# Kernel tuning notes

Measured on AMD Instinct MI355X. Metric: run time of the kernel, lower is better.

The kernel has to match this reference:

```python
import jax, jax.numpy as jnp
import numpy as np

PSIZE = 3
PSTRIDE = 3
N = PSIZE * PSTRIDE   # 9 attention tokens
P = PSIZE ** 2        # 9 pixels per token


def setup_inputs() -> dict:
    key = jax.random.key(0)
    k1, k2, k3, k4, k5 = jax.random.split(key, 5)
    B, H, W, C = 8192, 9, 9, 256
    hidden = C // 2
    x = jax.random.normal(k1, (B, H, W, C), dtype=jnp.float32)
    W_fc = jax.random.normal(k2, (hidden, C), dtype=jnp.float32) * (C ** -0.5)
    b_fc = jax.random.normal(k3, (hidden,), dtype=jnp.float32) * 0.01
    block_idx = jax.random.randint(k4, (B,), 0, 1024, dtype=jnp.int32)
    match_vec = jax.random.randint(k5, (1024, 1), 0, 2, dtype=jnp.int32)
    return {"x": x, "W_fc": W_fc, "b_fc": b_fc, "block_idx": block_idx, "match_vec": match_vec}


def reference(x, W_fc, b_fc, block_idx, match_vec):
    B, H, Wd, C = x.shape
    hidden = W_fc.shape[0]
    scale = (hidden * P) ** -0.5

    # [B, pstride, psize, pstride, psize, C] -> patch-major [B, ps, ps, p, p, C]
    xv = x.reshape(B, PSTRIDE, PSIZE, PSTRIDE, PSIZE, C).transpose(0, 1, 3, 2, 4, 5)
    x_fc = xv.reshape(B, N, P, C)

    # linear projection C -> hidden, then flatten pixels: q [B, N, P*hidden]
    q = (jnp.einsum('bnpc,hc->bnph', x_fc, W_fc) + b_fc).reshape(B, N, P * hidden)

    attn = jnp.einsum('bnd,bmd->bnm', q, q) * scale  # [B, N, N]

    # additive mask: -100 on diagonal, zeroed out entirely for matched samples
    base = jnp.where(jnp.eye(N, dtype=bool), jnp.float32(-100.0), jnp.float32(0.0))
    cur_match = match_vec[block_idx].squeeze(-1)  # [B]
    mask = jnp.where(cur_match[:, None, None] == 1, jnp.float32(0.0), base[None])

    attn = jax.nn.softmax(attn + mask, axis=-1)

    v = xv.reshape(B, N, P * C)
    out = attn @ v  # [B, N, P*C]

    out = out.reshape(B, PSTRIDE, PSTRIDE, PSIZE, PSIZE, C)
    out = out.transpose(0, 1, 3, 2, 4, 5).reshape(B, H, Wd, C)
    return out
```

## Files before the change

### kernel.cpp

```cpp
#include <hip/hip_runtime.h>

typedef short short8 __attribute__((ext_vector_type(8)));
typedef float floatx16 __attribute__((ext_vector_type(16)));
typedef float floatx4 __attribute__((ext_vector_type(4)));

#define ROWS 81
#define CDIM 256
#define XT   0
#define QH   41472
#define SC   51840
#define AB   52864
#define TOT  53376

__device__ __forceinline__ unsigned short f2bf(float f) {
    union { float f; unsigned int u; } v; v.f = f;
    return (unsigned short)((v.u + 0x7FFFu + ((v.u >> 16) & 1u)) >> 16);
}

__global__ void wconv_kernel(const float* __restrict__ W,
                             unsigned short* __restrict__ Wb, int n) {
    int i = blockIdx.x * 256 + threadIdx.x;
    if (i < n) Wb[i] = f2bf(W[i]);
}

__global__ __launch_bounds__(512, 6)
void attn_kernel(const float* __restrict__ x,
                 const unsigned short* __restrict__ Wb,
                 const float* __restrict__ b_fc,
                 const int* __restrict__ block_idx,
                 const int* __restrict__ match_vec,
                 float* __restrict__ out)
{
    __shared__ __align__(16) char smem[TOT];
    const int b     = blockIdx.x;
    const int t     = threadIdx.x;
    const int lane  = t & 63;
    const int wave  = t >> 6;
    const int l15   = lane & 15;
    const int kg    = lane >> 4;
    const int l31   = lane & 31;
    const int khalf = lane >> 5;

    int cm = 0;
    if (t < 9) cm = match_vec[block_idx[b]];

    short8 wfrag[8];
    {
        const unsigned short* wr = Wb + (wave * 16 + l15) * CDIM + kg * 8;
#pragma unroll
        for (int ks = 0; ks < 8; ++ks)
            wfrag[ks] = *(const short8*)(wr + ks * 32);
    }
    const float bias = b_fc[wave * 16 + l15];

    if (t < 256) ((float*)(smem + SC))[t] = 0.f;

    {
        const float* xb = x + (size_t)b * (ROWS * CDIM);
        for (int k = t; k < ROWS * 32; k += 512) {
            int gr = k >> 5;
            int c0 = (k & 31) * 8;
            float4 a0 = *(const float4*)(xb + gr * CDIM + c0);
            float4 a1 = *(const float4*)(xb + gr * CDIM + c0 + 4);
            int hh = gr / 9, ww = gr - hh * 9;
            int p = (hh % 3) * 3 + (ww % 3);
            int m = (hh / 3) * 3 + (ww / 3);
            int r = p * 9 + m;
            short8 v;
            v[0] = (short)f2bf(a0.x); v[1] = (short)f2bf(a0.y);
            v[2] = (short)f2bf(a0.z); v[3] = (short)f2bf(a0.w);
            v[4] = (short)f2bf(a1.x); v[5] = (short)f2bf(a1.y);
            v[6] = (short)f2bf(a1.z); v[7] = (short)f2bf(a1.w);
            *(short8*)(smem + XT + r * 512 + ((c0 * 2) ^ ((r & 15) << 4))) = v;
        }
    }
    __syncthreads();

    floatx4 acc[6];
#pragma unroll
    for (int i = 0; i < 6; ++i)
#pragma unroll
        for (int j = 0; j < 4; ++j) acc[i][j] = 0.f;
    const int swl = l15 << 4;
#pragma unroll
    for (int ks = 0; ks < 8; ++ks) {
        int cb = ks * 64 + kg * 16;
#pragma unroll
        for (int tile = 0; tile < 6; ++tile) {
            int r = tile * 16 + l15;
            short8 a = *(const short8*)(smem + XT + r * 512 + (cb ^ swl));
            acc[tile] = __builtin_amdgcn_mfma_f32_16x16x32_bf16(a, wfrag[ks], acc[tile], 0, 0, 0);
        }
    }

    if (wave < 4) {
        int h2 = (wave * 16 + l15) * 2;
#pragma unroll
        for (int tile = 0; tile < 6; ++tile)
#pragma unroll
            for (int reg = 0; reg < 4; ++reg) {
                int r = tile * 16 + kg * 4 + reg;
                if (r < ROWS)
                    *(unsigned short*)(smem + QH + r * 128 + (h2 ^ ((r & 7) << 4))) =
                        f2bf(acc[tile][reg] + bias);
            }
    }
    __syncthreads();

    const int nc = (l15 < 9) ? l15 : 8;
#define GRAM_HALF()                                                                 \
    {                                                                               \
        floatx4 g; g[0] = 0.f; g[1] = 0.f; g[2] = 0.f; g[3] = 0.f;                  \
        for (int ks = wave; ks < 18; ks += 8) {                                     \
            int p  = ks >> 1;                                                       \
            int h0 = (ks & 1) * 64 + kg * 16;           \
            int row = p * 9 + nc;                                                   \
            short8 f = *(const short8*)(smem + QH + row * 128 +                     \
                                        (h0 ^ ((row & 7) << 4)));                   \
            g = __builtin_amdgcn_mfma_f32_16x16x32_bf16(f, f, g, 0, 0, 0);          \
        }                                                                           \
        float* sc = (float*)(smem + SC);                                            \
        _Pragma("unroll")                                                           \
        for (int reg = 0; reg < 4; ++reg)                                           \
            atomicAdd(&sc[(kg * 4 + reg) * 16 + l15], g[reg]);                      \
    }
    GRAM_HALF();
    __syncthreads();

    if (wave >= 4) {
        int h2 = ((wave - 4) * 16 + l15) * 2;
#pragma unroll
        for (int tile = 0; tile < 6; ++tile)
#pragma unroll
            for (int reg = 0; reg < 4; ++reg) {
                int r = tile * 16 + kg * 4 + reg;
                if (r < ROWS)
                    *(unsigned short*)(smem + QH + r * 128 + (h2 ^ ((r & 7) << 4))) =
                        f2bf(acc[tile][reg] + bias);
            }
    }
    __syncthreads();
    GRAM_HALF();
    __syncthreads();

    if (t < 9) {
        const float scale = 0.029462782549439483f;
        float* sc = (float*)(smem + SC);
        float s[9];
        float mx = -1e30f;
#pragma unroll
        for (int m = 0; m < 9; ++m) {
            float v = sc[t * 16 + m] * scale;
            if (m == t && cm != 1) v -= 100.f;
            s[m] = v;
            mx = fmaxf(mx, v);
        }
        float sum = 0.f;
#pragma unroll
        for (int m = 0; m < 9; ++m) { s[m] = __expf(s[m] - mx); sum += s[m]; }
        float inv = 1.f / sum;
        unsigned short* ab = (unsigned short*)(smem + AB) + t * 16;
#pragma unroll
        for (int m = 0; m < 9; ++m) ab[m] = f2bf(s[m] * inv);
#pragma unroll
        for (int m = 9; m < 16; ++m) ab[m] = 0;
    }
    __syncthreads();

    {
        const int n  = l31;
        const int nm = (n < 9) ? n : 0;
        short8 bf = *(const short8*)(smem + AB + nm * 32 + khalf * 16);
        float* ob = out + (size_t)b * (ROWS * CDIM);
        int hh0 = 0, ww0 = 0;
        if (n < 9) { hh0 = (n / 3) * 3; ww0 = (n % 3) * 3; }
#pragma unroll
        for (int tt = 0; tt < 9; ++tt) {
            int tile = wave * 9 + tt;
            int d = tile * 32 + l31;
            int p = d >> 8, c = d & 255;
            short8 af;
#pragma unroll
            for (int j = 0; j < 8; ++j) {
                int mm = khalf * 8 + j; if (mm > 8) mm = 8;
                int row = p * 9 + mm;
                af[j] = *(const short*)(smem + XT + row * 512 + ((c * 2) ^ ((row & 15) << 4)));
            }
            floatx16 dacc;
#pragma unroll
            for (int i = 0; i < 16; ++i) dacc[i] = 0.f;
            dacc = __builtin_amdgcn_mfma_f32_32x32x16_bf16(af, bf, dacc, 0, 0, 0);
            if (n < 9) {
#pragma unroll
                for (int q2 = 0; q2 < 4; ++q2) {
                    int d0 = tile * 32 + q2 * 8 + khalf * 4;
                    int p0 = d0 >> 8, c0 = d0 & 255;
                    int gr = (hh0 + p0 / 3) * 9 + (ww0 + p0 % 3);
                    *(float4*)(ob + gr * CDIM + c0) =
                        make_float4(dacc[q2 * 4 + 0], dacc[q2 * 4 + 1],
                                    dacc[q2 * 4 + 2], dacc[q2 * 4 + 3]);
                }
            }
        }
    }
}

extern "C" void kernel_launch(void* const* d_in, const int* in_sizes, int n_in,
                              void* d_out, int out_size, void* d_ws, size_t ws_size,
                              hipStream_t stream) {
    const float* x    = (const float*)d_in[0];
    const float* W    = (const float*)d_in[1];
    const float* bfc  = (const float*)d_in[2];
    const int*   bidx = (const int*)d_in[3];
    const int*   mvec = (const int*)d_in[4];
    float* outp = (float*)d_out;
    unsigned short* Wb = (unsigned short*)d_ws;

    int nW = in_sizes[1];
    wconv_kernel<<<(nW + 255) / 256, 256, 0, stream>>>(W, Wb, nW);

    int B = in_sizes[0] / (ROWS * CDIM);
    attn_kernel<<<B, 512, 0, stream>>>(x, Wb, bfc, bidx, mvec, outp);
}
```

Before: 417.3 us.

## Store full Q tile at once, split Gram into per-wave partials, change swizzle

Enlarges the Q shared-memory region so all 8 waves write their projection results at once, removing the two-phase write/Gram sequence and two barriers. The Gram matrix is now computed by 4 waves, each writing its own partial buffer; the softmax thread sums the four partials, replacing the shared-memory atomics. The X-tile swizzle gains an extra XOR term to reduce bank conflicts, and the launch-bounds occupancy hint drops from 6 to 2 because shared-memory use per block grows to about 70 KB. Fewer blocks may fit per CU, which could reduce latency hiding in exchange for fewer barriers.

```diff
diff --git a/kernel.cpp b/kernel.cpp
--- a/kernel.cpp
+++ b/kernel.cpp
@@ -7,10 +7,12 @@
 #define ROWS 81
 #define CDIM 256
 #define XT   0
-#define QH   41472
-#define SC   51840
-#define AB   52864
-#define TOT  53376
+#define QT   41472
+#define SC   66048
+#define AB   70144
+#define TOT  70656
+
+#define SWX(r) ((((r) & 15) << 4) ^ (((r) & 8) << 3))
 
 __device__ __forceinline__ unsigned short f2bf(float f) {
     union { float f; unsigned int u; } v; v.f = f;
@@ -23,7 +25,7 @@
     if (i < n) Wb[i] = f2bf(W[i]);
 }
 
-__global__ __launch_bounds__(512, 6)
+__global__ __launch_bounds__(512, 2)
 void attn_kernel(const float* __restrict__ x,
                  const unsigned short* __restrict__ Wb,
                  const float* __restrict__ b_fc,
@@ -53,8 +55,6 @@
     }
     const float bias = b_fc[wave * 16 + l15];
 
-    if (t < 256) ((float*)(smem + SC))[t] = 0.f;
-
     {
         const float* xb = x + (size_t)b * (ROWS * CDIM);
         for (int k = t; k < ROWS * 32; k += 512) {
@@ -71,86 +71,73 @@
             v[2] = (short)f2bf(a0.z); v[3] = (short)f2bf(a0.w);
             v[4] = (short)f2bf(a1.x); v[5] = (short)f2bf(a1.y);
             v[6] = (short)f2bf(a1.z); v[7] = (short)f2bf(a1.w);
-            *(short8*)(smem + XT + r * 512 + ((c0 * 2) ^ ((r & 15) << 4))) = v;
-        }
-    }
-    __syncthreads();
-
-    floatx4 acc[6];
-#pragma unroll
-    for (int i = 0; i < 6; ++i)
-#pragma unroll
-        for (int j = 0; j < 4; ++j) acc[i][j] = 0.f;
-    const int swl = l15 << 4;
-#pragma unroll
-    for (int ks = 0; ks < 8; ++ks) {
-        int cb = ks * 64 + kg * 16;
-#pragma unroll
-        for (int tile = 0; tile < 6; ++tile) {
-            int r = tile * 16 + l15;
-            short8 a = *(const short8*)(smem + XT + r * 512 + (cb ^ swl));
-            acc[tile] = __builtin_amdgcn_mfma_f32_16x16x32_bf16(a, wfrag[ks], acc[tile], 0, 0, 0);
-        }
-    }
-
-    if (wave < 4) {
+            *(short8*)(smem + XT + r * 512 + ((c0 * 2) ^ SWX(r))) = v;
+        }
+    }
+    __syncthreads();
+
+    {
+        floatx4 acc[6];
+#pragma unroll
+        for (int ii = 0; ii < 6; ++ii)
+#pragma unroll
+            for (int j = 0; j < 4; ++j) acc[ii][j] = 0.f;
+#pragma unroll
+        for (int ks = 0; ks < 8; ++ks) {
+            int cb = ks * 64 + kg * 16;
+#pragma unroll
+            for (int tile = 0; tile < 6; ++tile) {
+                int r = tile * 16 + l15;
+                short8 a = *(const short8*)(smem + XT + r * 512 + (cb ^ SWX(r)));
+                acc[tile] = __builtin_amdgcn_mfma_f32_16x16x32_bf16(a, wfrag[ks], acc[tile], 0, 0, 0);
+            }
+        }
         int h2 = (wave * 16 + l15) * 2;
 #pragma unroll
         for (int tile = 0; tile < 6; ++tile)
 #pragma unroll
             for (int reg = 0; reg < 4; ++reg) {
                 int r = tile * 16 + kg * 4 + reg;
-                if (r < ROWS)
-                    *(unsigned short*)(smem + QH + r * 128 + (h2 ^ ((r & 7) << 4))) =
-                        f2bf(acc[tile][reg] + bias);
-            }
-    }
-    __syncthreads();
-
-    const int nc = (l15 < 9) ? l15 : 8;
-#define GRAM_HALF()                                                                 \
-    {                                                                               \
-        floatx4 g; g[0] = 0.f; g[1] = 0.f; g[2] = 0.f; g[3] = 0.f;                  \
-        for (int ks = wave; ks < 18; ks += 8) {                                     \
-            int p  = ks >> 1;                                                       \
-            int h0 = (ks & 1) * 64 + kg * 16;           \
-            int row = p * 9 + nc;                                                   \
-            short8 f = *(const short8*)(smem + QH + row * 128 +                     \
-                                        (h0 ^ ((row & 7) << 4)));                   \
-            g = __builtin_amdgcn_mfma_f32_16x16x32_bf16(f, f, g, 0, 0, 0);          \
-        }                                                                           \
-        float* sc = (float*)(smem + SC);                                            \
-        _Pragma("unroll")                                                           \
-        for (int reg = 0; reg < 4; ++reg)                                           \
-            atomicAdd(&sc[(kg * 4 + reg) * 16 + l15], g[reg]);                      \
-    }
-    GRAM_HALF();
-    __syncthreads();
-
-    if (wave >= 4) {
-        int h2 = ((wave - 4) * 16 + l15) * 2;
-#pragma unroll
-        for (int tile = 0; tile < 6; ++tile)
-#pragma unroll
-            for (int reg = 0; reg < 4; ++reg) {
-                int r = tile * 16 + kg * 4 + reg;
-                if (r < ROWS)
-                    *(unsigned short*)(smem + QH + r * 128 + (h2 ^ ((r & 7) << 4))) =
-                        f2bf(acc[tile][reg] + bias);
-            }
-    }
-    __syncthreads();
-    GRAM_HALF();
+                *(unsigned short*)(smem + QT + r * 256 + (h2 ^ ((r & 15) << 4))) =
+                    f2bf(acc[tile][reg] + bias);
+            }
+    }
+    __syncthreads();
+
+    if (wave < 4) {
+        floatx4 g;
+#pragma unroll
+        for (int ii = 0; ii < 4; ++ii) g[ii] = 0.f;
+        int nc = (l15 < 9) ? l15 : 8;
+#pragma unroll
+        for (int s = 0; s < 9; ++s) {
+            int ks = wave + s * 4;
+            int kk = ks * 32 + kg * 8;
+            int p  = kk >> 7;
+            int h0 = (kk & 127) * 2;
+            int row = p * 9 + nc;
+            short8 f = *(const short8*)(smem + QT + row * 256 + (h0 ^ ((row & 15) << 4)));
+            g = __builtin_amdgcn_mfma_f32_16x16x32_bf16(f, f, g, 0, 0, 0);
+        }
+        float* sc = (float*)(smem + SC + wave * 1024);
+#pragma unroll
+        for (int reg = 0; reg < 4; ++reg)
+            sc[(kg * 4 + reg) * 16 + l15] = g[reg];
+    }
     __syncthreads();
 
     if (t < 9) {
         const float scale = 0.029462782549439483f;
-        float* sc = (float*)(smem + SC);
+        const float* sc0 = (const float*)(smem + SC);
+        const float* sc1 = (const float*)(smem + SC + 1024);
+        const float* sc2 = (const float*)(smem + SC + 2048);
+        const float* sc3 = (const float*)(smem + SC + 3072);
         float s[9];
         float mx = -1e30f;
 #pragma unroll
         for (int m = 0; m < 9; ++m) {
-            float v = sc[t * 16 + m] * scale;
+            int o = t * 16 + m;
+            float v = (sc0[o] + sc1[o] + sc2[o] + sc3[o]) * scale;
             if (m == t && cm != 1) v -= 100.f;
             s[m] = v;
             mx = fmaxf(mx, v);
@@ -171,31 +158,30 @@
         const int n  = l31;
         const int nm = (n < 9) ? n : 0;
         short8 bf = *(const short8*)(smem + AB + nm * 32 + khalf * 16);
+        floatx16 zero16;
+#pragma unroll
+        for (int ii = 0; ii < 16; ++ii) zero16[ii] = 0.f;
         float* ob = out + (size_t)b * (ROWS * CDIM);
-        int hh0 = 0, ww0 = 0;
-        if (n < 9) { hh0 = (n / 3) * 3; ww0 = (n % 3) * 3; }
+        int hh = 0, ww = 0;
+        if (n < 9) { hh = (n / 3) * 3; ww = (n % 3) * 3; }
 #pragma unroll
         for (int tt = 0; tt < 9; ++tt) {
             int tile = wave * 9 + tt;
-            int d = tile * 32 + l31;
-            int p = d >> 8, c = d & 255;
+            int p = tile >> 3;
+            int c = (tile & 7) * 32 + l31;
             short8 af;
 #pragma unroll
             for (int j = 0; j < 8; ++j) {
                 int mm = khalf * 8 + j; if (mm > 8) mm = 8;
                 int row = p * 9 + mm;
-                af[j] = *(const short*)(smem + XT + row * 512 + ((c * 2) ^ ((row & 15) << 4)));
-            }
-            floatx16 dacc;
-#pragma unroll
-            for (int i = 0; i < 16; ++i) dacc[i] = 0.f;
-            dacc = __builtin_amdgcn_mfma_f32_32x32x16_bf16(af, bf, dacc, 0, 0, 0);
+                af[j] = *(const short*)(smem + XT + row * 512 + ((c * 2) ^ SWX(row)));
+            }
+            floatx16 dacc = __builtin_amdgcn_mfma_f32_32x32x16_bf16(af, bf, zero16, 0, 0, 0);
             if (n < 9) {
 #pragma unroll
                 for (int q2 = 0; q2 < 4; ++q2) {
-                    int d0 = tile * 32 + q2 * 8 + khalf * 4;
-                    int p0 = d0 >> 8, c0 = d0 & 255;
-                    int gr = (hh0 + p0 / 3) * 9 + (ww0 + p0 % 3);
+                    int c0 = (tile & 7) * 32 + q2 * 8 + khalf * 4;
+                    int gr = (hh + p / 3) * 9 + (ww + p % 3);
                     *(float4*)(ob + gr * CDIM + c0) =
                         make_float4(dacc[q2 * 4 + 0], dacc[q2 * 4 + 1],
                                     dacc[q2 * 4 + 2], dacc[q2 * 4 + 3]);
```

Result: faster. 365.5 us (-12.4%).
